# Kernel optimization log

Measured on AMD Instinct MI355X. Metric: run time of the kernel, lower is better.

## Reference

```python
import jax, jax.numpy as jnp
from jax import lax
import numpy as np

SEQ, B, H = 512, 64, 1024


def setup_inputs() -> dict:
    key = jax.random.key(0)
    k1, k2, k3, k4, k5, k6 = jax.random.split(key, 6)
    hidden = jax.random.normal(k1, (SEQ, B, H), dtype=jnp.float32)
    problem_q = jax.random.normal(k2, (B, H), dtype=jnp.float32)
    s = 1.0 / np.sqrt(H)
    WK = jax.random.uniform(k3, (H, H), minval=-s, maxval=s, dtype=jnp.float32)
    bK = jax.random.uniform(k4, (H,), minval=-s, maxval=s, dtype=jnp.float32)
    WV = jax.random.uniform(k5, (H, H), minval=-s, maxval=s, dtype=jnp.float32)
    bV = jax.random.uniform(k6, (H,), minval=-s, maxval=s, dtype=jnp.float32)
    return {"num_xs": 8, "hidden": hidden, "problem_q": problem_q,
            "WK": WK, "bK": bK, "WV": WV, "bV": bV}


def reference(num_xs, hidden, problem_q, WK, bK, WV, bV):
    # hidden: [S, B, H] -> [B, S, H]
    h = jnp.transpose(hidden, (1, 0, 2))
    k = jnp.einsum('bsh,kh->bsk', h, WK) + bK   # K projection, [B, S, H]
    v = jnp.einsum('bsh,vh->bsv', h, WV) + bV   # V projection, [B, S, H]

    def step(x, _):
        # x: [B, H]; scores over seq positions
        scores = jnp.einsum('bh,bsh->bs', x, k)       # [B, S]
        attn = jax.nn.softmax(scores, axis=-1)
        nx = jnp.einsum('bs,bsh->bh', attn, v)        # [B, H]
        return nx, nx

    _, rest = lax.scan(step, problem_q, None, length=num_xs - 1)  # [num_xs-1, B, H]
    xs = jnp.concatenate([problem_q[None], rest], axis=0)          # [num_xs, B, H]
    return jnp.transpose(xs, (1, 0, 2))                            # [B, num_xs, H]
```

## Files before the change

kernel.cpp:

```cpp
#include <hip/hip_runtime.h>

#define SEQ   512
#define BATCH 64
#define HID   1024
#define NX    8
#define SG    8
#define SB    8
#define NBAT  8

__global__ __launch_bounds__(256) void transpose_k(
    const float* __restrict__ in, float* __restrict__ outT)
{
    __shared__ float tile[32][33];
    const int bx = blockIdx.x * 32, by = blockIdx.y * 32;
    const int tx = threadIdx.x & 31, ty = threadIdx.x >> 5;
    #pragma unroll
    for (int r = ty; r < 32; r += 8)
        tile[r][tx] = in[(size_t)(by + r) * HID + bx + tx];
    __syncthreads();
    #pragma unroll
    for (int r = ty; r < 32; r += 8)
        outT[(size_t)(bx + r) * HID + by + tx] = tile[tx][r];
}

__global__ __launch_bounds__(256) void wc_gemm(
    const float* __restrict__ WV, const float* __restrict__ WK,
    float* __restrict__ WC)
{
    __shared__ float As[32][68];
    __shared__ float Bs[32][68];
    const int nt = blockIdx.x, mt = blockIdx.y;
    const int tid = threadIdx.x;
    const int nx = tid & 15, my = tid >> 4;

    const int r = tid >> 3, c = (tid & 7) * 8;

    float acc[4][4] = {};

    float4 a0 = *(const float4*)(WV + (size_t)(0 + r) * HID + mt * 64 + c);
    float4 a1 = *(const float4*)(WV + (size_t)(0 + r) * HID + mt * 64 + c + 4);
    float4 b0 = *(const float4*)(WK + (size_t)(0 + r) * HID + nt * 64 + c);
    float4 b1 = *(const float4*)(WK + (size_t)(0 + r) * HID + nt * 64 + c + 4);

    for (int k0 = 0; k0 < HID; k0 += 32) {
        *(float4*)&As[r][c]     = a0;
        *(float4*)&As[r][c + 4] = a1;
        *(float4*)&Bs[r][c]     = b0;
        *(float4*)&Bs[r][c + 4] = b1;
        __syncthreads();

        if (k0 + 32 < HID) {
            a0 = *(const float4*)(WV + (size_t)(k0 + 32 + r) * HID + mt * 64 + c);
            a1 = *(const float4*)(WV + (size_t)(k0 + 32 + r) * HID + mt * 64 + c + 4);
            b0 = *(const float4*)(WK + (size_t)(k0 + 32 + r) * HID + nt * 64 + c);
            b1 = *(const float4*)(WK + (size_t)(k0 + 32 + r) * HID + nt * 64 + c + 4);
        }

        #pragma unroll 8
        for (int kk = 0; kk < 32; kk++) {
            const float4 a = *(const float4*)&As[kk][my * 4];
            const float4 b = *(const float4*)&Bs[kk][nx * 4];
            acc[0][0] += a.x * b.x; acc[0][1] += a.x * b.y;
            acc[0][2] += a.x * b.z; acc[0][3] += a.x * b.w;
            acc[1][0] += a.y * b.x; acc[1][1] += a.y * b.y;
            acc[1][2] += a.y * b.z; acc[1][3] += a.y * b.w;
            acc[2][0] += a.z * b.x; acc[2][1] += a.z * b.y;
            acc[2][2] += a.z * b.z; acc[2][3] += a.z * b.w;
            acc[3][0] += a.w * b.x; acc[3][1] += a.w * b.y;
            acc[3][2] += a.w * b.z; acc[3][3] += a.w * b.w;
        }
        __syncthreads();
    }

    const int m = mt * 64 + my * 4, n = nt * 64 + nx * 4;
    #pragma unroll
    for (int i = 0; i < 4; i++)
        *(float4*)(WC + (size_t)(m + i) * HID + n) = *(float4*)acc[i];
}

__global__ __launch_bounds__(256) void y_kernel(
    const float* __restrict__ W, const float* __restrict__ q,
    const float* __restrict__ zp, const float* __restrict__ ml,
    const float* __restrict__ bc, float* __restrict__ zs_slot,
    float* __restrict__ y, int mode)
{
    __shared__ float xs[HID];
    __shared__ float red[8][32];
    const int nc = blockIdx.x, b = blockIdx.y;
    const int tid = threadIdx.x;

    if (mode == 0) {
        *(float4*)(xs + tid * 4) = *(const float4*)(q + (size_t)b * HID + tid * 4);
    } else {
        float M = -1e30f;
        #pragma unroll
        for (int g = 0; g < SG; g++) M = fmaxf(M, ml[b * 2 * SG + 2 * g]);
        float es[SG], L = 0.f;
        #pragma unroll
        for (int g = 0; g < SG; g++) {
            es[g] = __expf(ml[b * 2 * SG + 2 * g] - M);
            L += ml[b * 2 * SG + 2 * g + 1] * es[g];
        }
        const float invL = 1.0f / L;
        for (int i = tid; i < HID; i += 256) {
            float s = 0.f;
            #pragma unroll
            for (int g = 0; g < SG; g++)
                s += zp[((size_t)(b * SG + g)) * HID + i] * es[g];
            s *= invL;
            xs[i] = s;
            if (nc == 0 && zs_slot) zs_slot[(size_t)b * HID + i] = s;
        }
    }
    __syncthreads();

    const int nl = tid & 31, jg = tid >> 5;
    const int n = nc * 32 + nl;
    const float* __restrict__ wp = W + (size_t)(jg * 128) * HID + n;
    const float* __restrict__ xr = xs + jg * 128;
    float acc = 0.f;
    #pragma unroll 8
    for (int jj = 0; jj < 128; jj++)
        acc += xr[jj] * wp[(size_t)jj * HID];
    red[jg][nl] = acc;
    __syncthreads();
    if (tid < 32) {
        float s = 0.f;
        #pragma unroll
        for (int g = 0; g < 8; g++) s += red[g][tid];
        if (mode != 0) s += bc[nc * 32 + tid];
        y[(size_t)b * HID + nc * 32 + tid] = s;
    }
}

__global__ __launch_bounds__(256) void fused_attn_kernel(
    const float* __restrict__ hidden, const float* __restrict__ y,
    float* __restrict__ zp, float* __restrict__ ml)
{
    const int sg = blockIdx.x, b = blockIdx.y;
    const int tid = threadIdx.x;
    const int lane = tid & 63, w = tid >> 6;
    const int h4 = tid * 4;

    __shared__ float part[4][SB];

    const float4 yv = *(const float4*)(y + (size_t)b * HID + h4);
    float m = -1e30f, l = 0.f;
    float4 acc = {0.f, 0.f, 0.f, 0.f};

    for (int bb = 0; bb < NBAT; bb++) {
        float4 hv[SB];
        float p[SB];
        #pragma unroll
        for (int r = 0; r < SB; r++) {
            const int s = sg * 64 + bb * SB + r;
            hv[r] = *(const float4*)(hidden + ((size_t)s * BATCH + b) * HID + h4);
            p[r] = hv[r].x * yv.x + hv[r].y * yv.y
                 + hv[r].z * yv.z + hv[r].w * yv.w;
        }
        #pragma unroll
        for (int r = 0; r < SB; r++) {
            float s = p[r];
            #pragma unroll
            for (int off = 32; off; off >>= 1) s += __shfl_xor(s, off);
            if (lane == 0) part[w][r] = s;
        }
        __syncthreads();
        float sc[SB], mb = -1e30f;
        #pragma unroll
        for (int r = 0; r < SB; r++) {
            sc[r] = part[0][r] + part[1][r] + part[2][r] + part[3][r];
            mb = fmaxf(mb, sc[r]);
        }
        __syncthreads();
        const float newm  = fmaxf(m, mb);
        const float scale = __expf(m - newm);
        l *= scale;
        acc.x *= scale; acc.y *= scale; acc.z *= scale; acc.w *= scale;
        #pragma unroll
        for (int r = 0; r < SB; r++) {
            const float we = __expf(sc[r] - newm);
            l += we;
            acc.x += we * hv[r].x; acc.y += we * hv[r].y;
            acc.z += we * hv[r].z; acc.w += we * hv[r].w;
        }
        m = newm;
    }
    *(float4*)(zp + ((size_t)(b * SG + sg)) * HID + h4) = acc;
    if (tid == 0) {
        ml[(b * SG + sg) * 2 + 0] = m;
        ml[(b * SG + sg) * 2 + 1] = l;
    }
}

__global__ __launch_bounds__(256) void final_gemm(
    const float* __restrict__ WVT, const float* __restrict__ zs,
    const float* __restrict__ zp, const float* __restrict__ ml,
    const float* __restrict__ q, const float* __restrict__ bV,
    float* __restrict__ out)
{
    __shared__ float zst[7][HID];
    __shared__ float red[8][7][32];
    const int nc = blockIdx.x, b = blockIdx.y;
    const int tid = threadIdx.x;

    float M = -1e30f;
    #pragma unroll
    for (int g = 0; g < SG; g++) M = fmaxf(M, ml[b * 2 * SG + 2 * g]);
    float es[SG], L = 0.f;
    #pragma unroll
    for (int g = 0; g < SG; g++) {
        es[g] = __expf(ml[b * 2 * SG + 2 * g] - M);
        L += ml[b * 2 * SG + 2 * g + 1] * es[g];
    }
    const float invL = 1.0f / L;

    for (int i = tid; i < 7 * HID; i += 256) {
        const int si = i >> 10;
        const int h  = i & (HID - 1);
        float v;
        if (si < 6) {
            v = zs[((size_t)si * BATCH + b) * HID + h];
        } else {
            v = 0.f;
            #pragma unroll
            for (int g = 0; g < SG; g++)
                v += zp[((size_t)(b * SG + g)) * HID + h] * es[g];
            v *= invL;
        }
        zst[si][h] = v;
    }
    __syncthreads();

    const int nl = tid & 31, hg = tid >> 5;
    const int n = nc * 32 + nl;
    const float* __restrict__ wp = WVT + (size_t)(hg * 128) * HID + n;
    float acc[7] = {};
    #pragma unroll 4
    for (int hh = 0; hh < 128; hh++) {
        const float wv = wp[(size_t)hh * HID];
        const int h = hg * 128 + hh;
        #pragma unroll
        for (int si = 0; si < 7; si++)
            acc[si] += zst[si][h] * wv;
    }
    #pragma unroll
    for (int si = 0; si < 7; si++) red[hg][si][nl] = acc[si];
    __syncthreads();

    if (tid < 224) {
        const int si = tid >> 5, nl2 = tid & 31;
        const int n2 = nc * 32 + nl2;
        float s = bV[n2];
        #pragma unroll
        for (int g = 0; g < 8; g++) s += red[g][si][nl2];
        out[((size_t)(b * NX + si + 1)) * HID + n2] = s;
    } else {
        const int nl2 = tid - 224;
        const int n2 = nc * 32 + nl2;
        out[((size_t)(b * NX)) * HID + n2] = q[(size_t)b * HID + n2];
    }
}

extern "C" void kernel_launch(void* const* d_in, const int* in_sizes, int n_in,
                              void* d_out, int out_size, void* d_ws, size_t ws_size,
                              hipStream_t stream)
{
    const float* hidden = (const float*)d_in[1];
    const float* q      = (const float*)d_in[2];
    const float* WK     = (const float*)d_in[3];
    const float* WV     = (const float*)d_in[5];
    const float* bV     = (const float*)d_in[6];
    float* out = (float*)d_out;

    char* ws = (char*)d_ws;
    float* WVT = (float*)(ws);
    float* WC  = (float*)(ws + (4  << 20));
    float* zp  = (float*)(ws + (8  << 20));
    float* zs  = (float*)(ws + (10 << 20));
    float* y   = (float*)(ws + (12 << 20));
    float* ml  = (float*)(ws + (12 << 20) + (256 << 10));
    float* bc  = (float*)(ws + (12 << 20) + (512 << 10));

    transpose_k<<<dim3(32, 32), 256, 0, stream>>>(WV, WVT);
    wc_gemm<<<dim3(16, 16), 256, 0, stream>>>(WV, WK, WC);
    y_kernel<<<dim3(32, 1), 256, 0, stream>>>(
        WK, bV, nullptr, nullptr, nullptr, nullptr, bc, 0);

    for (int t = 1; t < NX; t++) {
        if (t == 1) {
            y_kernel<<<dim3(32, BATCH), 256, 0, stream>>>(
                WK, q, nullptr, nullptr, nullptr, nullptr, y, 0);
        } else {
            float* slot = zs + (size_t)(t - 2) * BATCH * HID;
            y_kernel<<<dim3(32, BATCH), 256, 0, stream>>>(
                WC, nullptr, zp, ml, bc, slot, y, 1);
        }
        fused_attn_kernel<<<dim3(SG, BATCH), 256, 0, stream>>>(
            hidden, y, zp, ml);
    }
    final_gemm<<<dim3(32, BATCH), 256, 0, stream>>>(
        WVT, zs, zp, ml, q, bV, out);
}
```

Baseline: 372.4 us.

## Merge setup kernels into one launch and swap grid axes for weight reuse

The WV transpose, the WC=WV·WK GEMM and the bias projection bc now run as one kernel, each part picked by block-index range. This removes two launches and lets the three independent setup jobs run at the same time. The y_kernel and final_gemm grids also swap axes so batch is the fast dimension. Consecutive blocks then share the same weight column chunk, which should improve L2 reuse of the weights. The merged kernel sizes shared memory for the largest part, which may lower occupancy for the lighter transpose blocks.

```diff
diff --git a/kernel.cpp b/kernel.cpp
--- a/kernel.cpp
+++ b/kernel.cpp
@@ -8,74 +8,94 @@
 #define SB    8
 #define NBAT  8
 
-__global__ __launch_bounds__(256) void transpose_k(
-    const float* __restrict__ in, float* __restrict__ outT)
-{
-    __shared__ float tile[32][33];
-    const int bx = blockIdx.x * 32, by = blockIdx.y * 32;
-    const int tx = threadIdx.x & 31, ty = threadIdx.x >> 5;
-    #pragma unroll
-    for (int r = ty; r < 32; r += 8)
-        tile[r][tx] = in[(size_t)(by + r) * HID + bx + tx];
-    __syncthreads();
-    #pragma unroll
-    for (int r = ty; r < 32; r += 8)
-        outT[(size_t)(bx + r) * HID + by + tx] = tile[tx][r];
-}
-
-__global__ __launch_bounds__(256) void wc_gemm(
+__global__ __launch_bounds__(256) void init_kernel(
     const float* __restrict__ WV, const float* __restrict__ WK,
-    float* __restrict__ WC)
-{
-    __shared__ float As[32][68];
-    __shared__ float Bs[32][68];
-    const int nt = blockIdx.x, mt = blockIdx.y;
+    const float* __restrict__ bV, float* __restrict__ WVT,
+    float* __restrict__ WC, float* __restrict__ bc)
+{
+    __shared__ float smem[2 * 32 * 68];
+    const int bid = blockIdx.x;
     const int tid = threadIdx.x;
-    const int nx = tid & 15, my = tid >> 4;
-
-    const int r = tid >> 3, c = (tid & 7) * 8;
-
-    float acc[4][4] = {};
-
-    float4 a0 = *(const float4*)(WV + (size_t)(0 + r) * HID + mt * 64 + c);
-    float4 a1 = *(const float4*)(WV + (size_t)(0 + r) * HID + mt * 64 + c + 4);
-    float4 b0 = *(const float4*)(WK + (size_t)(0 + r) * HID + nt * 64 + c);
-    float4 b1 = *(const float4*)(WK + (size_t)(0 + r) * HID + nt * 64 + c + 4);
-
-    for (int k0 = 0; k0 < HID; k0 += 32) {
-        *(float4*)&As[r][c]     = a0;
-        *(float4*)&As[r][c + 4] = a1;
-        *(float4*)&Bs[r][c]     = b0;
-        *(float4*)&Bs[r][c + 4] = b1;
-        __syncthreads();
-
-        if (k0 + 32 < HID) {
-            a0 = *(const float4*)(WV + (size_t)(k0 + 32 + r) * HID + mt * 64 + c);
-            a1 = *(const float4*)(WV + (size_t)(k0 + 32 + r) * HID + mt * 64 + c + 4);
-            b0 = *(const float4*)(WK + (size_t)(k0 + 32 + r) * HID + nt * 64 + c);
-            b1 = *(const float4*)(WK + (size_t)(k0 + 32 + r) * HID + nt * 64 + c + 4);
-        }
-
+
+    if (bid < 256) {
+        float (*As)[68] = (float(*)[68])smem;
+        float (*Bs)[68] = (float(*)[68])(smem + 32 * 68);
+        const int nt = bid & 15, mt = bid >> 4;
+        const int nx = tid & 15, my = tid >> 4;
+        const int r = tid >> 3, c = (tid & 7) * 8;
+
+        float acc[4][4] = {};
+        float4 a0 = *(const float4*)(WV + (size_t)r * HID + mt * 64 + c);
+        float4 a1 = *(const float4*)(WV + (size_t)r * HID + mt * 64 + c + 4);
+        float4 b0 = *(const float4*)(WK + (size_t)r * HID + nt * 64 + c);
+        float4 b1 = *(const float4*)(WK + (size_t)r * HID + nt * 64 + c + 4);
+
+        for (int k0 = 0; k0 < HID; k0 += 32) {
+            *(float4*)&As[r][c]     = a0;
+            *(float4*)&As[r][c + 4] = a1;
+            *(float4*)&Bs[r][c]     = b0;
+            *(float4*)&Bs[r][c + 4] = b1;
+            __syncthreads();
+            if (k0 + 32 < HID) {
+                a0 = *(const float4*)(WV + (size_t)(k0 + 32 + r) * HID + mt * 64 + c);
+                a1 = *(const float4*)(WV + (size_t)(k0 + 32 + r) * HID + mt * 64 + c + 4);
+                b0 = *(const float4*)(WK + (size_t)(k0 + 32 + r) * HID + nt * 64 + c);
+                b1 = *(const float4*)(WK + (size_t)(k0 + 32 + r) * HID + nt * 64 + c + 4);
+            }
+            #pragma unroll 8
+            for (int kk = 0; kk < 32; kk++) {
+                const float4 a = *(const float4*)&As[kk][my * 4];
+                const float4 b = *(const float4*)&Bs[kk][nx * 4];
+                acc[0][0] += a.x * b.x; acc[0][1] += a.x * b.y;
+                acc[0][2] += a.x * b.z; acc[0][3] += a.x * b.w;
+                acc[1][0] += a.y * b.x; acc[1][1] += a.y * b.y;
+                acc[1][2] += a.y * b.z; acc[1][3] += a.y * b.w;
+                acc[2][0] += a.z * b.x; acc[2][1] += a.z * b.y;
+                acc[2][2] += a.z * b.z; acc[2][3] += a.z * b.w;
+                acc[3][0] += a.w * b.x; acc[3][1] += a.w * b.y;
+                acc[3][2] += a.w * b.z; acc[3][3] += a.w * b.w;
+            }
+            __syncthreads();
+        }
+        const int m = mt * 64 + my * 4, n = nt * 64 + nx * 4;
+        #pragma unroll
+        for (int i = 0; i < 4; i++)
+            *(float4*)(WC + (size_t)(m + i) * HID + n) = *(float4*)acc[i];
+    } else if (bid < 1280) {
+        float (*tile)[33] = (float(*)[33])smem;
+        const int idx = bid - 256;
+        const int bx = (idx & 31) * 32, by = (idx >> 5) * 32;
+        const int tx = tid & 31, ty = tid >> 5;
+        #pragma unroll
+        for (int r2 = ty; r2 < 32; r2 += 8)
+            tile[r2][tx] = WV[(size_t)(by + r2) * HID + bx + tx];
+        __syncthreads();
+        #pragma unroll
+        for (int r2 = ty; r2 < 32; r2 += 8)
+            WVT[(size_t)(bx + r2) * HID + by + tx] = tile[tx][r2];
+    } else {
+        float* xs  = smem;
+        float* red = smem + 1024;
+        const int nc = bid - 1280;
+        *(float4*)(xs + tid * 4) = *(const float4*)(bV + tid * 4);
+        __syncthreads();
+        const int nl = tid & 31, jg = tid >> 5;
+        const int n = nc * 32 + nl;
+        const float* __restrict__ wp = WK + (size_t)(jg * 128) * HID + n;
+        const float* __restrict__ xr = xs + jg * 128;
+        float acc = 0.f;
         #pragma unroll 8
-        for (int kk = 0; kk < 32; kk++) {
-            const float4 a = *(const float4*)&As[kk][my * 4];
-            const float4 b = *(const float4*)&Bs[kk][nx * 4];
-            acc[0][0] += a.x * b.x; acc[0][1] += a.x * b.y;
-            acc[0][2] += a.x * b.z; acc[0][3] += a.x * b.w;
-            acc[1][0] += a.y * b.x; acc[1][1] += a.y * b.y;
-            acc[1][2] += a.y * b.z; acc[1][3] += a.y * b.w;
-            acc[2][0] += a.z * b.x; acc[2][1] += a.z * b.y;
-            acc[2][2] += a.z * b.z; acc[2][3] += a.z * b.w;
-            acc[3][0] += a.w * b.x; acc[3][1] += a.w * b.y;
-            acc[3][2] += a.w * b.z; acc[3][3] += a.w * b.w;
-        }
-        __syncthreads();
-    }
-
-    const int m = mt * 64 + my * 4, n = nt * 64 + nx * 4;
-    #pragma unroll
-    for (int i = 0; i < 4; i++)
-        *(float4*)(WC + (size_t)(m + i) * HID + n) = *(float4*)acc[i];
+        for (int jj = 0; jj < 128; jj++)
+            acc += xr[jj] * wp[(size_t)jj * HID];
+        red[jg * 32 + nl] = acc;
+        __syncthreads();
+        if (tid < 32) {
+            float s = 0.f;
+            #pragma unroll
+            for (int g = 0; g < 8; g++) s += red[g * 32 + tid];
+            bc[nc * 32 + tid] = s;
+        }
+    }
 }
 
 __global__ __launch_bounds__(256) void y_kernel(
@@ -86,7 +106,7 @@
 {
     __shared__ float xs[HID];
     __shared__ float red[8][32];
-    const int nc = blockIdx.x, b = blockIdx.y;
+    const int b = blockIdx.x, nc = blockIdx.y;
     const int tid = threadIdx.x;
 
     if (mode == 0) {
@@ -201,7 +221,7 @@
 {
     __shared__ float zst[7][HID];
     __shared__ float red[8][7][32];
-    const int nc = blockIdx.x, b = blockIdx.y;
+    const int b = blockIdx.x, nc = blockIdx.y;
     const int tid = threadIdx.x;
 
     float M = -1e30f;
@@ -282,23 +302,20 @@
     float* ml  = (float*)(ws + (12 << 20) + (256 << 10));
     float* bc  = (float*)(ws + (12 << 20) + (512 << 10));
 
-    transpose_k<<<dim3(32, 32), 256, 0, stream>>>(WV, WVT);
-    wc_gemm<<<dim3(16, 16), 256, 0, stream>>>(WV, WK, WC);
-    y_kernel<<<dim3(32, 1), 256, 0, stream>>>(
-        WK, bV, nullptr, nullptr, nullptr, nullptr, bc, 0);
+    init_kernel<<<1312, 256, 0, stream>>>(WV, WK, bV, WVT, WC, bc);
 
     for (int t = 1; t < NX; t++) {
         if (t == 1) {
-            y_kernel<<<dim3(32, BATCH), 256, 0, stream>>>(
+            y_kernel<<<dim3(BATCH, 32), 256, 0, stream>>>(
                 WK, q, nullptr, nullptr, nullptr, nullptr, y, 0);
         } else {
             float* slot = zs + (size_t)(t - 2) * BATCH * HID;
-            y_kernel<<<dim3(32, BATCH), 256, 0, stream>>>(
+            y_kernel<<<dim3(BATCH, 32), 256, 0, stream>>>(
                 WC, nullptr, zp, ml, bc, slot, y, 1);
         }
         fused_attn_kernel<<<dim3(SG, BATCH), 256, 0, stream>>>(
             hidden, y, zp, ml);
     }
-    final_gemm<<<dim3(32, BATCH), 256, 0, stream>>>(
+    final_gemm<<<dim3(BATCH, 32), 256, 0, stream>>>(
         WVT, zs, zp, ml, q, bV, out);
 }
```

Measured after the change: 390.8 us. 1.05x slower.
